# Optimization experiments

Measured on AMD Instinct MI355X. Metric: run time of the kernel, lower is better.

## Reference

```python
import jax, jax.numpy as jnp
import numpy as np

B, TQ, TK, E, H, DH = 4, 1024, 1024, 1024, 16, 64
EPS = 1e-5

def setup_inputs() -> dict:
    key = jax.random.key(0)
    ks = jax.random.split(key, 16)
    s = 0.02
    return {
        "x": jax.random.normal(ks[0], (B, TQ, E), jnp.float32),
        "encoder_out": jax.random.normal(ks[1], (B, TK, E), jnp.float32),
        "Q1w": jax.random.normal(ks[2], (H, DH, E), jnp.float32) * s,
        "Q1b": jax.random.normal(ks[3], (H, DH), jnp.float32) * s,
        "Q2w": jax.random.normal(ks[4], (H, DH, E), jnp.float32) * s,
        "Q2b": jax.random.normal(ks[5], (H, DH), jnp.float32) * s,
        "K1w": jax.random.normal(ks[6], (H, DH, E), jnp.float32) * s,
        "K1b": jax.random.normal(ks[7], (H, DH), jnp.float32) * s,
        "K2w": jax.random.normal(ks[8], (H, DH, E), jnp.float32) * s,
        "K2b": jax.random.normal(ks[9], (H, DH), jnp.float32) * s,
        "Vw": jax.random.normal(ks[10], (H, DH, E), jnp.float32) * s,
        "Vb": jax.random.normal(ks[11], (H, DH), jnp.float32) * s,
        "lam": jax.random.uniform(ks[12], (H,), jnp.float32, 0.5, 1.0),
        "gn_gamma": jnp.ones((H * DH,), jnp.float32),
        "gn_beta": jnp.zeros((H * DH,), jnp.float32),
        "out_w": jax.random.normal(ks[13], (E, H * DH), jnp.float32) * s,
        "out_b": jax.random.normal(ks[14], (E,), jnp.float32) * s,
    }

def _proj(inp, w, b):
    # inp: [B,T,E], w: [H,DH,E] -> [B,H,T,DH]
    return jnp.einsum('bte,hde->bhtd', inp, w) + b[None, :, None, :]

def reference(x, encoder_out, Q1w, Q1b, Q2w, Q2b, K1w, K1b, K2w, K2b, Vw, Vb,
              lam, gn_gamma, gn_beta, out_w, out_b):
    scale = 1.0 / jnp.sqrt(jnp.float32(DH))
    q1 = _proj(x, Q1w, Q1b)
    q2 = _proj(x, Q2w, Q2b)
    k1 = _proj(encoder_out, K1w, K1b)
    k2 = _proj(encoder_out, K2w, K2b)
    v = _proj(encoder_out, Vw, Vb)
    s1 = jnp.einsum('bhtd,bhsd->bhts', q1, k1) * scale  # [B,H,TQ,TK]
    s2 = jnp.einsum('bhtd,bhsd->bhts', q2, k2) * scale
    w = jax.nn.softmax(s1, axis=-1) - lam[None, :, None, None] * jax.nn.softmax(s2, axis=-1)
    out = jnp.einsum('bhts,bhsd->bhtd', w, v)  # [B,H,TQ,DH]
    # GroupNorm(num_groups=H, channels=H*DH) over [B,C,T]: per (B,H) stats over (T,DH)
    mu = jnp.mean(out, axis=(2, 3), keepdims=True)
    var = jnp.mean(jnp.square(out - mu), axis=(2, 3), keepdims=True)
    normed = (out - mu) * jax.lax.rsqrt(var + EPS)
    g = gn_gamma.reshape(H, DH)[None, :, None, :]
    b_ = gn_beta.reshape(H, DH)[None, :, None, :]
    normed = normed * g + b_
    y = normed.transpose(0, 2, 1, 3).reshape(B, TQ, H * DH)
    return y @ out_w.T + out_b
```

## Files before the change

### kernel.cpp

```cpp
#include <hip/hip_runtime.h>
#include <cmath>

typedef __bf16 bf16_t;
typedef bf16_t bf16x8 __attribute__((ext_vector_type(8)));
typedef bf16_t bf16x4 __attribute__((ext_vector_type(4)));
typedef float  f32x4  __attribute__((ext_vector_type(4)));
typedef float  f32x16 __attribute__((ext_vector_type(16)));
typedef unsigned int u32x4v __attribute__((ext_vector_type(4)));

#define Bn  4
#define TQn 1024
#define TKn 1024
#define En  1024
#define Hn  16
#define DHn 64

static constexpr float EPSv = 1e-5f;
static constexpr float C_SCALE = 0.18033688011112042f;

#define GLDS16(g, l)                                                         \
    __builtin_amdgcn_global_load_lds(                                        \
        (const __attribute__((address_space(1))) void*)(g),                  \
        (__attribute__((address_space(3))) void*)(l), 16, 0, 0)

__global__ __launch_bounds__(256)
void cvt_all(const float* __restrict__ x, const float* __restrict__ enc,
             const float* __restrict__ q1w, const float* __restrict__ q2w,
             const float* __restrict__ k1w, const float* __restrict__ k2w,
             const float* __restrict__ vw,  const float* __restrict__ outw,
             bf16_t* __restrict__ xb, bf16_t* __restrict__ encb,
             bf16_t* __restrict__ wq, bf16_t* __restrict__ wkv,
             bf16_t* __restrict__ wob)
{
    int idx = blockIdx.x * 256 + threadIdx.x;
    const float* src; bf16_t* dst;
    if      (idx < 1048576) { src = x    + (size_t)idx * 4;              dst = xb   + (size_t)idx * 4; }
    else if (idx < 2097152) { src = enc  + (size_t)(idx - 1048576) * 4;  dst = encb + (size_t)(idx - 1048576) * 4; }
    else if (idx < 2359296) { src = q1w  + (size_t)(idx - 2097152) * 4;  dst = wq   + (size_t)(idx - 2097152) * 4; }
    else if (idx < 2621440) { src = q2w  + (size_t)(idx - 2359296) * 4;  dst = wq   + 1048576 + (size_t)(idx - 2359296) * 4; }
    else if (idx < 2883584) { src = k1w  + (size_t)(idx - 2621440) * 4;  dst = wkv  + (size_t)(idx - 2621440) * 4; }
    else if (idx < 3145728) { src = k2w  + (size_t)(idx - 2883584) * 4;  dst = wkv  + 1048576 + (size_t)(idx - 2883584) * 4; }
    else if (idx < 3407872) { src = vw   + (size_t)(idx - 3145728) * 4;  dst = wkv  + 2097152 + (size_t)(idx - 3145728) * 4; }
    else                    { src = outw + (size_t)(idx - 3407872) * 4;  dst = wob  + (size_t)(idx - 3407872) * 4; }
    float4 v = *(const float4*)src;
    bf16x4 o;
    o[0] = (bf16_t)v.x; o[1] = (bf16_t)v.y; o[2] = (bf16_t)v.z; o[3] = (bf16_t)v.w;
    *(bf16x4*)dst = o;
}

__global__ __launch_bounds__(256, 3)
void gemm_proj(const bf16_t* __restrict__ xb, const bf16_t* __restrict__ encb,
               const bf16_t* __restrict__ wq, const bf16_t* __restrict__ wkv,
               const float* __restrict__ q1b, const float* __restrict__ q2b,
               const float* __restrict__ k1b, const float* __restrict__ k2b,
               const float* __restrict__ vb,
               bf16_t* __restrict__ q12, bf16_t* __restrict__ k12v)
{
    __shared__ __align__(16) bf16_t sAB[2][128 * 64];
    bf16_t* const sA = &sAB[0][0];
    bf16_t* const sB = &sAB[1][0];
    bf16_t* const sC = &sAB[0][0];

    int bx = blockIdx.x;
    const int blockM = blockIdx.y << 7;
    const bf16_t* A; const bf16_t* W; bf16_t* C; const float* bp; int blockN;
    if (bx < 16) {
        A = xb; W = wq; C = q12; blockN = bx << 7;
        bp = (blockN >> 10) ? q2b : q1b;
    } else {
        bx -= 16;
        A = encb; W = wkv; C = k12v; blockN = bx << 7;
        const int seg0 = blockN >> 10;
        bp = (seg0 == 0) ? k1b : ((seg0 == 1) ? k2b : vb);
    }

    const int tid = threadIdx.x;
    const int w = tid >> 6, lane = tid & 63;
    const int q = lane >> 4, r = lane & 15;
    const int wm = w & 1, wn = w >> 1;

    f32x4 acc[4][4];
#pragma unroll
    for (int i = 0; i < 4; ++i)
#pragma unroll
        for (int j = 0; j < 4; ++j) acc[i][j] = (f32x4){0.f, 0.f, 0.f, 0.f};

    for (int k0 = 0; k0 < 1024; k0 += 64) {
#pragma unroll
        for (int c = 0; c < 4; ++c) {
            const int s = c * 256 + tid;
            const int row = s >> 3;
            const int cg = (s & 7) ^ (row & 7);
            GLDS16(A + (size_t)(blockM + row) * 1024 + k0 + cg * 8, sA + c * 2048 + w * 512);
            GLDS16(W + (size_t)(blockN + row) * 1024 + k0 + cg * 8, sB + c * 2048 + w * 512);
        }
        __syncthreads();
#pragma unroll
        for (int ks = 0; ks < 2; ++ks) {
            bf16x8 a[4], b[4];
#pragma unroll
            for (int i = 0; i < 4; ++i) {
                const int row = wm * 64 + i * 16 + r;
                const int g = (ks * 4 + q) ^ (row & 7);
                a[i] = *(const bf16x8*)&sA[row * 64 + g * 8];
            }
#pragma unroll
            for (int j = 0; j < 4; ++j) {
                const int row = wn * 64 + j * 16 + r;
                const int g = (ks * 4 + q) ^ (row & 7);
                b[j] = *(const bf16x8*)&sB[row * 64 + g * 8];
            }
#pragma unroll
            for (int i = 0; i < 4; ++i)
#pragma unroll
                for (int j = 0; j < 4; ++j)
                    acc[i][j] = __builtin_amdgcn_mfma_f32_16x16x32_bf16(a[i], b[j], acc[i][j], 0, 0, 0);
        }
        __syncthreads();
    }

#pragma unroll
    for (int j = 0; j < 4; ++j) {
        const int n = wn * 64 + j * 16 + r;
        const float bv = bp[(blockN + n) & 1023];
#pragma unroll
        for (int i = 0; i < 4; ++i) {
            f32x4 v = acc[i][j];
#pragma unroll
            for (int e = 0; e < 4; ++e) {
                const int m = wm * 64 + i * 16 + q * 4 + e;
                sC[m * 128 + (((n >> 3) ^ (m & 7)) << 3) + (n & 7)] = (bf16_t)(v[e] + bv);
            }
        }
    }
    __syncthreads();
    const int seg = blockN >> 10;
#pragma unroll
    for (int v8 = 0; v8 < 8; ++v8) {
        const int flat = v8 * 256 + tid;
        const int m = flat >> 4;
        const int nb = flat & 15;
        bf16x8 row = *(const bf16x8*)&sC[m * 128 + ((nb ^ (m & 7)) << 3)];
        const int gm = blockM + m, gn = blockN + nb * 8;
        const int bb = gm >> 10, t = gm & 1023;
        const int h = (gn >> 6) & 15, d = gn & 63;
        *(bf16x8*)&C[((((size_t)seg * 4 + bb) * 16 + h) * 1024 + t) * 64 + d] = row;
    }
}

__global__ __launch_bounds__(256, 4)
void gemm_out(const bf16_t* __restrict__ yb, const bf16_t* __restrict__ wob,
              const float* __restrict__ outb, float* __restrict__ out)
{
    __shared__ bf16_t sA[64 * 64];
    __shared__ bf16_t sB[128 * 64];
    const int L = blockIdx.x;
    const int xcd = L & 7, kk = L >> 3;
    const int blockM = (xcd * 8 + (kk >> 3)) * 64;
    const int blockN = (kk & 7) * 128;

    const int tid = threadIdx.x;
    const int w = tid >> 6, lane = tid & 63;
    const int q = lane >> 4, r = lane & 15;

    f32x4 acc[4][2];
#pragma unroll
    for (int i = 0; i < 4; ++i)
#pragma unroll
        for (int j = 0; j < 2; ++j) acc[i][j] = (f32x4){0.f, 0.f, 0.f, 0.f};

    for (int k0 = 0; k0 < 1024; k0 += 64) {
#pragma unroll
        for (int c = 0; c < 2; ++c) {
            const int s = c * 256 + tid;
            const int row = s >> 3;
            const int cg = (s & 7) ^ (row & 7);
            GLDS16(yb + (size_t)(blockM + row) * 1024 + k0 + cg * 8, sA + c * 2048 + w * 512);
        }
#pragma unroll
        for (int c = 0; c < 4; ++c) {
            const int s = c * 256 + tid;
            const int row = s >> 3;
            const int cg = (s & 7) ^ (row & 7);
            GLDS16(wob + (size_t)(blockN + row) * 1024 + k0 + cg * 8, sB + c * 2048 + w * 512);
        }
        __syncthreads();
#pragma unroll
        for (int ks = 0; ks < 2; ++ks) {
            bf16x8 a[4], b[2];
#pragma unroll
            for (int i = 0; i < 4; ++i) {
                const int row = i * 16 + r;
                const int g = (ks * 4 + q) ^ (row & 7);
                a[i] = *(const bf16x8*)&sA[row * 64 + g * 8];
            }
#pragma unroll
            for (int j = 0; j < 2; ++j) {
                const int row = w * 32 + j * 16 + r;
                const int g = (ks * 4 + q) ^ (row & 7);
                b[j] = *(const bf16x8*)&sB[row * 64 + g * 8];
            }
#pragma unroll
            for (int i = 0; i < 4; ++i)
#pragma unroll
                for (int j = 0; j < 2; ++j)
                    acc[i][j] = __builtin_amdgcn_mfma_f32_16x16x32_bf16(a[i], b[j], acc[i][j], 0, 0, 0);
        }
        __syncthreads();
    }

#pragma unroll
    for (int j = 0; j < 2; ++j) {
        const int n = blockN + w * 32 + j * 16 + r;
        const float bv = outb[n];
#pragma unroll
        for (int i = 0; i < 4; ++i) {
            f32x4 v = acc[i][j];
#pragma unroll
            for (int e = 0; e < 4; ++e) {
                const int m = blockM + i * 16 + q * 4 + e;
                out[(size_t)m * 1024 + n] = v[e] + bv;
            }
        }
    }
}

__device__ __forceinline__ unsigned cvtpk_bf16(float a, float b)
{
    unsigned r;
    asm("v_cvt_pk_bf16_f32 %0, %1, %2" : "=v"(r) : "v"(a), "v"(b));
    return r;
}

__device__ __forceinline__ void pack_pa(const f32x16& p, bf16x8& pa0, bf16x8& pa1)
{
    unsigned a0 = cvtpk_bf16(p[0], p[1]),   b0 = cvtpk_bf16(p[4], p[5]);
    asm("v_permlane32_swap_b32 %0, %1" : "+v"(a0), "+v"(b0));
    unsigned a1 = cvtpk_bf16(p[2], p[3]),   b1 = cvtpk_bf16(p[6], p[7]);
    asm("v_permlane32_swap_b32 %0, %1" : "+v"(a1), "+v"(b1));
    pa0 = __builtin_bit_cast(bf16x8, (u32x4v){a0, a1, b0, b1});
    unsigned a2 = cvtpk_bf16(p[8], p[9]),   b2 = cvtpk_bf16(p[12], p[13]);
    asm("v_permlane32_swap_b32 %0, %1" : "+v"(a2), "+v"(b2));
    unsigned a3 = cvtpk_bf16(p[10], p[11]), b3 = cvtpk_bf16(p[14], p[15]);
    asm("v_permlane32_swap_b32 %0, %1" : "+v"(a3), "+v"(b3));
    pa1 = __builtin_bit_cast(bf16x8, (u32x4v){a2, a3, b2, b3});
}

__global__ __launch_bounds__(512, 4)
void diff_attn32(const bf16_t* __restrict__ q12, const bf16_t* __restrict__ k12v,
                 const float* __restrict__ lam, bf16_t* __restrict__ out,
                 float* __restrict__ stats)
{
    __shared__ __align__(16) bf16_t arena[20480];
    bf16_t* const sK1 = arena;
    bf16_t* const sK2 = arena + 8192;
    bf16_t* const sVt = arena + 16384;
    float*  const xchg = (float*)arena;
    __shared__ float sl[2][128];
    __shared__ float sred[16];

    const int tid = threadIdx.x;
    const int w = tid >> 6, lane = tid & 63;
    const int st_id = w >> 2, wv = w & 3;
    const int hi = lane >> 5, lo = lane & 31;
    const int bh = blockIdx.x, qt = blockIdx.y;
    const float lamv = lam[bh & (Hn - 1)];

    const size_t HT = (size_t)TKn * DHn;
    const bf16_t* qg  = q12 + (size_t)(st_id * 64 + bh) * HT + (size_t)qt * 128 * DHn;
    const bf16_t* k1g = k12v + (size_t)bh * HT;
    const bf16_t* k2g = k1g + 64 * HT;
    const bf16_t* vg  = k1g + 128 * HT;
    const bf16_t* const sKs = st_id ? sK2 : sK1;

    bf16x8 fQ[4];
#pragma unroll
    for (int dk = 0; dk < 4; ++dk)
        fQ[dk] = *(const bf16x8*)(qg + (size_t)(wv * 32 + lo) * 64 + dk * 16 + hi * 8);

    f32x16 O0, O1;
#pragma unroll
    for (int e = 0; e < 16; ++e) { O0[e] = 0.f; O1[e] = 0.f; }
    float lsum = 0.f;

    {
        const int row = tid >> 3;
        const int cg = (tid & 7) ^ (row & 7);
        GLDS16(k1g + row * 64 + cg * 8, sK1 + tid * 8);
        GLDS16(k2g + row * 64 + cg * 8, sK2 + tid * 8);
        const int s = tid & 63;
        bf16x8 v0 = *(const bf16x8*)(vg + (size_t)s * 64 + w * 8);
        __syncthreads();
#pragma unroll
        for (int i = 0; i < 8; ++i) {
            const int d = w * 8 + i;
            sVt[d * 64 + (((s >> 3) ^ i) << 3) + (s & 7)] = v0[i];
        }
        __syncthreads();
    }

    bf16x8 vr;
    for (int st = 0; st < TKn / 64; ++st) {
        const int cur = st & 1;
        if (st < 15) {
            const int row = tid >> 3;
            const int cg = (tid & 7) ^ (row & 7);
            GLDS16(k1g + (size_t)(st + 1) * 4096 + row * 64 + cg * 8, sK1 + (cur ^ 1) * 4096 + tid * 8);
            GLDS16(k2g + (size_t)(st + 1) * 4096 + row * 64 + cg * 8, sK2 + (cur ^ 1) * 4096 + tid * 8);
            vr = *(const bf16x8*)(vg + (size_t)(st + 1) * 4096 + (size_t)(tid & 63) * 64 + w * 8);
        }

        const bf16_t* sKc = sKs + cur * 4096;
#pragma unroll
        for (int kb = 0; kb < 2; ++kb) {
            f32x16 S;
#pragma unroll
            for (int e = 0; e < 16; ++e) S[e] = 0.f;
            __builtin_amdgcn_s_setprio(1);
#pragma unroll
            for (int dk = 0; dk < 4; ++dk) {
                bf16x8 fk = *(const bf16x8*)&sKc[(kb * 32 + lo) * 64 + (((dk * 2 + hi) ^ (lo & 7)) << 3)];
                S = __builtin_amdgcn_mfma_f32_32x32x16_bf16(fk, fQ[dk], S, 0, 0, 0);
            }
            __builtin_amdgcn_s_setprio(0);
#pragma unroll
            for (int e = 0; e < 16; ++e) {
                S[e] = __builtin_amdgcn_exp2f(S[e] * C_SCALE);
                lsum += S[e];
            }
            bf16x8 pa0, pa1;
            pack_pa(S, pa0, pa1);
            const int c0 = ((kb * 4 + 0 * 2 + hi) ^ (lo & 7)) << 3;
            const int c1 = ((kb * 4 + 1 * 2 + hi) ^ (lo & 7)) << 3;
            bf16x8 fv00 = *(const bf16x8*)&sVt[(0 * 32 + lo) * 64 + c0];
            bf16x8 fv01 = *(const bf16x8*)&sVt[(0 * 32 + lo) * 64 + c1];
            bf16x8 fv10 = *(const bf16x8*)&sVt[(1 * 32 + lo) * 64 + c0];
            bf16x8 fv11 = *(const bf16x8*)&sVt[(1 * 32 + lo) * 64 + c1];
            __builtin_amdgcn_s_setprio(1);
            O0 = __builtin_amdgcn_mfma_f32_32x32x16_bf16(pa0, fv00, O0, 0, 0, 0);
            O0 = __builtin_amdgcn_mfma_f32_32x32x16_bf16(pa1, fv01, O0, 0, 0, 0);
            O1 = __builtin_amdgcn_mfma_f32_32x32x16_bf16(pa0, fv10, O1, 0, 0, 0);
            O1 = __builtin_amdgcn_mfma_f32_32x32x16_bf16(pa1, fv11, O1, 0, 0, 0);
            __builtin_amdgcn_s_setprio(0);
        }

        __syncthreads();
        if (st < 15) {
            const int s = tid & 63;
#pragma unroll
            for (int i = 0; i < 8; ++i) {
                const int d = w * 8 + i;
                sVt[d * 64 + (((s >> 3) ^ i) << 3) + (s & 7)] = vr[i];
            }
            __syncthreads();
        }
    }

    lsum += __shfl_xor(lsum, 32);
    if (hi == 0) sl[st_id][wv * 32 + lo] = lsum;

    if (st_id == 1) {
#pragma unroll
        for (int reg = 0; reg < 16; ++reg) {
            const int t = wv * 32 + (reg & 3) + 8 * (reg >> 2) + 4 * hi;
            const float inv2 = lamv / sl[1][t];
            xchg[t * 64 + lo]      = O0[reg] * inv2;
            xchg[t * 64 + 32 + lo] = O1[reg] * inv2;
        }
    }
    __syncthreads();

    if (st_id == 0) {
        float ssum = 0.f, ssq = 0.f;
        bf16_t* op = out + ((size_t)bh * TQn + (size_t)qt * 128) * DHn;
#pragma unroll
        for (int reg = 0; reg < 16; ++reg) {
            const int t = wv * 32 + (reg & 3) + 8 * (reg >> 2) + 4 * hi;
            const float inv1 = 1.0f / sl[0][t];
            const float o0 = O0[reg] * inv1 - xchg[t * 64 + lo];
            const float o1 = O1[reg] * inv1 - xchg[t * 64 + 32 + lo];
            op[(size_t)t * 64 + lo]      = (bf16_t)o0;
            op[(size_t)t * 64 + 32 + lo] = (bf16_t)o1;
            ssum += o0 + o1;
            ssq  += o0 * o0 + o1 * o1;
        }
#pragma unroll
        for (int d = 1; d < 64; d <<= 1) {
            ssum += __shfl_xor(ssum, d);
            ssq  += __shfl_xor(ssq, d);
        }
        if (lane == 0) { sred[wv] = ssum; sred[8 + wv] = ssq; }
    }
    __syncthreads();
    if (tid == 0) {
        stats[(bh << 3) + qt]       = sred[0] + sred[1] + sred[2] + sred[3];
        stats[512 + (bh << 3) + qt] = sred[8] + sred[9] + sred[10] + sred[11];
    }
}

__global__ __launch_bounds__(256)
void gn_apply(const bf16_t* __restrict__ attn, const float* __restrict__ stats,
              const float* __restrict__ gamma, const float* __restrict__ beta,
              bf16_t* __restrict__ y)
{
    const int f = blockIdx.x * 256 + threadIdx.x;
    const int d8 = (f & 7) << 3;
    const int t  = (f >> 3) & 1023;
    const int bh = f >> 13;
    const int h  = bh & 15;
    const int b  = bh >> 4;
    const float* p1 = stats + (bh << 3);
    const float* p2 = stats + 512 + (bh << 3);
    float s1 = 0.f, s2 = 0.f;
#pragma unroll
    for (int k = 0; k < 8; ++k) { s1 += p1[k]; s2 += p2[k]; }
    const float mu = s1 * (1.f / 65536.f);
    const float var = s2 * (1.f / 65536.f) - mu * mu;
    const float rstd = rsqrtf(var + EPSv);
    bf16x8 v = *(const bf16x8*)&attn[((size_t)bh << 16) + t * 64 + d8];
    const int c = h * 64 + d8;
    const float* gp = gamma + c;
    const float* bp = beta + c;
    bf16x8 o;
#pragma unroll
    for (int i = 0; i < 8; ++i)
        o[i] = (bf16_t)(((float)v[i] - mu) * rstd * gp[i] + bp[i]);
    *(bf16x8*)&y[((size_t)(b * 1024 + t)) * 1024 + c] = o;
}

extern "C" void kernel_launch(void* const* d_in, const int* in_sizes, int n_in,
                              void* d_out, int out_size, void* d_ws, size_t ws_size,
                              hipStream_t stream)
{
    const float* x    = (const float*)d_in[0];
    const float* enc  = (const float*)d_in[1];
    const float* Q1w  = (const float*)d_in[2];
    const float* Q1b  = (const float*)d_in[3];
    const float* Q2w  = (const float*)d_in[4];
    const float* Q2b  = (const float*)d_in[5];
    const float* K1w  = (const float*)d_in[6];
    const float* K1b  = (const float*)d_in[7];
    const float* K2w  = (const float*)d_in[8];
    const float* K2b  = (const float*)d_in[9];
    const float* Vw   = (const float*)d_in[10];
    const float* Vb   = (const float*)d_in[11];
    const float* lam  = (const float*)d_in[12];
    const float* gng  = (const float*)d_in[13];
    const float* gnb  = (const float*)d_in[14];
    const float* outw = (const float*)d_in[15];
    const float* outb = (const float*)d_in[16];
    float* out = (float*)d_out;

    bf16_t* xb   = (bf16_t*)d_ws;
    bf16_t* encb = xb   + 4194304;
    bf16_t* wq   = encb + 4194304;
    bf16_t* wkv  = wq   + 2097152;
    bf16_t* wob  = wkv  + 3145728;
    bf16_t* q12  = wob  + 1048576;
    bf16_t* k12v = q12  + 8388608;
    bf16_t* attnb= xb;
    bf16_t* yb   = encb;
    float*  stats= (float*)wq;

    cvt_all<<<14336, 256, 0, stream>>>(x, enc, Q1w, Q2w, K1w, K2w, Vw, outw,
                                       xb, encb, wq, wkv, wob);

    gemm_proj<<<dim3(40, 32), 256, 0, stream>>>(xb, encb, wq, wkv,
                                                Q1b, Q2b, K1b, K2b, Vb, q12, k12v);

    diff_attn32<<<dim3(64, 8), 512, 0, stream>>>(q12, k12v, lam, attnb, stats);

    gn_apply<<<2048, 256, 0, stream>>>(attnb, stats, gng, gnb, yb);

    gemm_out<<<512, 256, 0, stream>>>(yb, wob, outb, out);
}
```

Measured before the change: 249.4 us.

## Fuse GroupNorm apply into output GEMM and double-buffer V in attention

Removes the separate gn_apply kernel. The output GEMM now computes per-head GroupNorm scale and shift from the stats and applies them while loading attention tiles into shared memory, which saves a full write and re-read of the normalized activations and one launch. The A-tile load changes from async global-to-LDS to register loads plus conversion, which may reduce latency hiding. The attention kernel double-buffers the transposed V tile so one barrier per iteration can be dropped, at the cost of more LDS. Launch bounds rise for gemm_proj and diff_attn32, which puts pressure on register allocation.

New measurement: 325.8 us. +30.6%, slower.

```diff
diff --git a/kernel.cpp b/kernel.cpp
--- a/kernel.cpp
+++ b/kernel.cpp
@@ -48,7 +48,7 @@
     *(bf16x4*)dst = o;
 }
 
-__global__ __launch_bounds__(256, 3)
+__global__ __launch_bounds__(256, 4)
 void gemm_proj(const bf16_t* __restrict__ xb, const bf16_t* __restrict__ encb,
                const bf16_t* __restrict__ wq, const bf16_t* __restrict__ wkv,
                const float* __restrict__ q1b, const float* __restrict__ q2b,
@@ -149,20 +149,48 @@
 }
 
 __global__ __launch_bounds__(256, 4)
-void gemm_out(const bf16_t* __restrict__ yb, const bf16_t* __restrict__ wob,
-              const float* __restrict__ outb, float* __restrict__ out)
-{
-    __shared__ bf16_t sA[64 * 64];
-    __shared__ bf16_t sB[128 * 64];
+void gemm_out_gn(const bf16_t* __restrict__ attnb, const float* __restrict__ stats,
+                 const float* __restrict__ gamma, const float* __restrict__ beta,
+                 const bf16_t* __restrict__ wob, const float* __restrict__ outb,
+                 float* __restrict__ out)
+{
+    __shared__ __align__(16) bf16_t sA[64 * 64];
+    __shared__ __align__(16) bf16_t sB[128 * 64];
+    __shared__ float sCa[1024];
+    __shared__ float sCb[1024];
+    __shared__ float sMu[16], sRs[16];
+
     const int L = blockIdx.x;
     const int xcd = L & 7, kk = L >> 3;
     const int blockM = (xcd * 8 + (kk >> 3)) * 64;
     const int blockN = (kk & 7) * 128;
+    const int b = blockM >> 10;
 
     const int tid = threadIdx.x;
     const int w = tid >> 6, lane = tid & 63;
     const int q = lane >> 4, r = lane & 15;
 
+    if (tid < 16) {
+        const int bh = b * 16 + tid;
+        float s1 = 0.f, s2 = 0.f;
+#pragma unroll
+        for (int k = 0; k < 8; ++k) { s1 += stats[bh * 8 + k]; s2 += stats[512 + bh * 8 + k]; }
+        const float mu = s1 * (1.f / 65536.f);
+        const float var = s2 * (1.f / 65536.f) - mu * mu;
+        sMu[tid] = mu;
+        sRs[tid] = rsqrtf(var + EPSv);
+    }
+    __syncthreads();
+#pragma unroll
+    for (int u = 0; u < 4; ++u) {
+        const int c = u * 256 + tid;
+        const int h = c >> 6;
+        const float a = sRs[h] * gamma[c];
+        sCa[c] = a;
+        sCb[c] = beta[c] - sMu[h] * a;
+    }
+    __syncthreads();
+
     f32x4 acc[4][2];
 #pragma unroll
     for (int i = 0; i < 4; ++i)
@@ -170,12 +198,26 @@
         for (int j = 0; j < 2; ++j) acc[i][j] = (f32x4){0.f, 0.f, 0.f, 0.f};
 
     for (int k0 = 0; k0 < 1024; k0 += 64) {
+        const int h = k0 >> 6;
 #pragma unroll
         for (int c = 0; c < 2; ++c) {
             const int s = c * 256 + tid;
             const int row = s >> 3;
-            const int cg = (s & 7) ^ (row & 7);
-            GLDS16(yb + (size_t)(blockM + row) * 1024 + k0 + cg * 8, sA + c * 2048 + w * 512);
+            const int cb = s & 7;
+            const int t = (blockM + row) & 1023;
+            bf16x8 v = *(const bf16x8*)(attnb + ((size_t)(b * 16 + h) << 16) + t * 64 + cb * 8);
+            const int cbase = h * 64 + cb * 8;
+            f32x4 ca0 = *(const f32x4*)&sCa[cbase];
+            f32x4 ca1 = *(const f32x4*)&sCa[cbase + 4];
+            f32x4 cb0 = *(const f32x4*)&sCb[cbase];
+            f32x4 cb1 = *(const f32x4*)&sCb[cbase + 4];
+            bf16x8 o;
+#pragma unroll
+            for (int i = 0; i < 4; ++i) {
+                o[i]     = (bf16_t)((float)v[i]     * ca0[i] + cb0[i]);
+                o[i + 4] = (bf16_t)((float)v[i + 4] * ca1[i] + cb1[i]);
+            }
+            *(bf16x8*)&sA[row * 64 + ((cb ^ (row & 7)) << 3)] = o;
         }
 #pragma unroll
         for (int c = 0; c < 4; ++c) {
@@ -187,7 +229,7 @@
         __syncthreads();
 #pragma unroll
         for (int ks = 0; ks < 2; ++ks) {
-            bf16x8 a[4], b[2];
+            bf16x8 a[4], bfr[2];
 #pragma unroll
             for (int i = 0; i < 4; ++i) {
                 const int row = i * 16 + r;
@@ -198,13 +240,13 @@
             for (int j = 0; j < 2; ++j) {
                 const int row = w * 32 + j * 16 + r;
                 const int g = (ks * 4 + q) ^ (row & 7);
-                b[j] = *(const bf16x8*)&sB[row * 64 + g * 8];
+                bfr[j] = *(const bf16x8*)&sB[row * 64 + g * 8];
             }
 #pragma unroll
             for (int i = 0; i < 4; ++i)
 #pragma unroll
                 for (int j = 0; j < 2; ++j)
-                    acc[i][j] = __builtin_amdgcn_mfma_f32_16x16x32_bf16(a[i], b[j], acc[i][j], 0, 0, 0);
+                    acc[i][j] = __builtin_amdgcn_mfma_f32_16x16x32_bf16(a[i], bfr[j], acc[i][j], 0, 0, 0);
         }
         __syncthreads();
     }
@@ -246,12 +288,12 @@
     pa1 = __builtin_bit_cast(bf16x8, (u32x4v){a2, a3, b2, b3});
 }
 
-__global__ __launch_bounds__(512, 4)
+__global__ __launch_bounds__(512, 6)
 void diff_attn32(const bf16_t* __restrict__ q12, const bf16_t* __restrict__ k12v,
                  const float* __restrict__ lam, bf16_t* __restrict__ out,
                  float* __restrict__ stats)
 {
-    __shared__ __align__(16) bf16_t arena[20480];
+    __shared__ __align__(16) bf16_t arena[24576];
     bf16_t* const sK1 = arena;
     bf16_t* const sK2 = arena + 8192;
     bf16_t* const sVt = arena + 16384;
@@ -290,7 +332,6 @@
         GLDS16(k2g + row * 64 + cg * 8, sK2 + tid * 8);
         const int s = tid & 63;
         bf16x8 v0 = *(const bf16x8*)(vg + (size_t)s * 64 + w * 8);
-        __syncthreads();
 #pragma unroll
         for (int i = 0; i < 8; ++i) {
             const int d = w * 8 + i;
@@ -299,18 +340,19 @@
         __syncthreads();
     }
 
-    bf16x8 vr;
     for (int st = 0; st < TKn / 64; ++st) {
-        const int cur = st & 1;
+        const int cur = st & 1, nxt = cur ^ 1;
+        bf16x8 vr;
         if (st < 15) {
             const int row = tid >> 3;
             const int cg = (tid & 7) ^ (row & 7);
-            GLDS16(k1g + (size_t)(st + 1) * 4096 + row * 64 + cg * 8, sK1 + (cur ^ 1) * 4096 + tid * 8);
-            GLDS16(k2g + (size_t)(st + 1) * 4096 + row * 64 + cg * 8, sK2 + (cur ^ 1) * 4096 + tid * 8);
+            GLDS16(k1g + (size_t)(st + 1) * 4096 + row * 64 + cg * 8, sK1 + nxt * 4096 + tid * 8);
+            GLDS16(k2g + (size_t)(st + 1) * 4096 + row * 64 + cg * 8, sK2 + nxt * 4096 + tid * 8);
             vr = *(const bf16x8*)(vg + (size_t)(st + 1) * 4096 + (size_t)(tid & 63) * 64 + w * 8);
         }
 
         const bf16_t* sKc = sKs + cur * 4096;
+        const bf16_t* sVc = sVt + cur * 4096;
 #pragma unroll
         for (int kb = 0; kb < 2; ++kb) {
             f32x16 S;
@@ -330,12 +372,12 @@
             }
             bf16x8 pa0, pa1;
             pack_pa(S, pa0, pa1);
-            const int c0 = ((kb * 4 + 0 * 2 + hi) ^ (lo & 7)) << 3;
-            const int c1 = ((kb * 4 + 1 * 2 + hi) ^ (lo & 7)) << 3;
-            bf16x8 fv00 = *(const bf16x8*)&sVt[(0 * 32 + lo) * 64 + c0];
-            bf16x8 fv01 = *(const bf16x8*)&sVt[(0 * 32 + lo) * 64 + c1];
-            bf16x8 fv10 = *(const bf16x8*)&sVt[(1 * 32 + lo) * 64 + c0];
-            bf16x8 fv11 = *(const bf16x8*)&sVt[(1 * 32 + lo) * 64 + c1];
+            const int c0 = ((kb * 4 + hi) ^ (lo & 7)) << 3;
+            const int c1 = ((kb * 4 + 2 + hi) ^ (lo & 7)) << 3;
+            bf16x8 fv00 = *(const bf16x8*)&sVc[(0 * 32 + lo) * 64 + c0];
+            bf16x8 fv01 = *(const bf16x8*)&sVc[(0 * 32 + lo) * 64 + c1];
+            bf16x8 fv10 = *(const bf16x8*)&sVc[(1 * 32 + lo) * 64 + c0];
+            bf16x8 fv11 = *(const bf16x8*)&sVc[(1 * 32 + lo) * 64 + c1];
             __builtin_amdgcn_s_setprio(1);
             O0 = __builtin_amdgcn_mfma_f32_32x32x16_bf16(pa0, fv00, O0, 0, 0, 0);
             O0 = __builtin_amdgcn_mfma_f32_32x32x16_bf16(pa1, fv01, O0, 0, 0, 0);
@@ -344,16 +386,15 @@
             __builtin_amdgcn_s_setprio(0);
         }
 
-        __syncthreads();
         if (st < 15) {
             const int s = tid & 63;
 #pragma unroll
             for (int i = 0; i < 8; ++i) {
                 const int d = w * 8 + i;
-                sVt[d * 64 + (((s >> 3) ^ i) << 3) + (s & 7)] = vr[i];
-            }
-            __syncthreads();
-        }
+                sVt[nxt * 4096 + d * 64 + (((s >> 3) ^ i) << 3) + (s & 7)] = vr[i];
+            }
+        }
+        __syncthreads();
     }
 
     lsum += __shfl_xor(lsum, 32);
@@ -396,36 +437,6 @@
         stats[(bh << 3) + qt]       = sred[0] + sred[1] + sred[2] + sred[3];
         stats[512 + (bh << 3) + qt] = sred[8] + sred[9] + sred[10] + sred[11];
     }
-}
-
-__global__ __launch_bounds__(256)
-void gn_apply(const bf16_t* __restrict__ attn, const float* __restrict__ stats,
-              const float* __restrict__ gamma, const float* __restrict__ beta,
-              bf16_t* __restrict__ y)
-{
-    const int f = blockIdx.x * 256 + threadIdx.x;
-    const int d8 = (f & 7) << 3;
-    const int t  = (f >> 3) & 1023;
-    const int bh = f >> 13;
-    const int h  = bh & 15;
-    const int b  = bh >> 4;
-    const float* p1 = stats + (bh << 3);
-    const float* p2 = stats + 512 + (bh << 3);
-    float s1 = 0.f, s2 = 0.f;
-#pragma unroll
-    for (int k = 0; k < 8; ++k) { s1 += p1[k]; s2 += p2[k]; }
-    const float mu = s1 * (1.f / 65536.f);
-    const float var = s2 * (1.f / 65536.f) - mu * mu;
-    const float rstd = rsqrtf(var + EPSv);
-    bf16x8 v = *(const bf16x8*)&attn[((size_t)bh << 16) + t * 64 + d8];
-    const int c = h * 64 + d8;
-    const float* gp = gamma + c;
-    const float* bp = beta + c;
-    bf16x8 o;
-#pragma unroll
-    for (int i = 0; i < 8; ++i)
-        o[i] = (bf16_t)(((float)v[i] - mu) * rstd * gp[i] + bp[i]);
-    *(bf16x8*)&y[((size_t)(b * 1024 + t)) * 1024 + c] = o;
 }
 
 extern "C" void kernel_launch(void* const* d_in, const int* in_sizes, int n_in,
@@ -459,7 +470,6 @@
     bf16_t* q12  = wob  + 1048576;
     bf16_t* k12v = q12  + 8388608;
     bf16_t* attnb= xb;
-    bf16_t* yb   = encb;
     float*  stats= (float*)wq;
 
     cvt_all<<<14336, 256, 0, stream>>>(x, enc, Q1w, Q2w, K1w, K2w, Vw, outw,
@@ -470,7 +480,5 @@
 
     diff_attn32<<<dim3(64, 8), 512, 0, stream>>>(q12, k12v, lam, attnb, stats);
 
-    gn_apply<<<2048, 256, 0, stream>>>(attnb, stats, gng, gnb, yb);
-
-    gemm_out<<<512, 256, 0, stream>>>(yb, wob, outb, out);
-}
+    gemm_out_gn<<<512, 256, 0, stream>>>(attnb, stats, gng, gnb, wob, outb, out);
+}
```
